# Kernel tuning notes

Hardware: AMD Instinct MI355X
Metric: run time of the kernel (lower is better)

The kernel has to match this reference:

```python
import jax, jax.numpy as jnp
import numpy as np

TOP_K = 2


def setup_inputs() -> dict:
    key = jax.random.key(0)
    k_x, k_g, k_w1, k_w2, k_w3 = jax.random.split(key, 5)
    B, S, D, H, E = 2, 512, 1024, 512, 8
    x = jax.random.normal(k_x, (B, S, D), dtype=jnp.float32)
    gate_w = jax.random.normal(k_g, (D, E), dtype=jnp.float32) * (D ** -0.5)
    w1 = jax.random.normal(k_w1, (E, D, H), dtype=jnp.float32) * 0.02  # gate proj
    w2 = jax.random.normal(k_w2, (E, H, D), dtype=jnp.float32) * 0.02  # down proj
    w3 = jax.random.normal(k_w3, (E, D, H), dtype=jnp.float32) * 0.02  # up proj
    return {"x": x, "gate_w": gate_w, "w1": w1, "w2": w2, "w3": w3}


def reference(x, gate_w, w1, w2, w3):
    # Token-choice top-k MoE with grouped SwiGLU experts, no shared expert.
    # Equivalent to torchtune MoE: gather routed tokens, scale by top-k router
    # score, run per-expert FFN, scatter-add back. Since each expert's FFN has
    # no bias (FFN(0) == 0), the dispatch/grouped-GEMM/combine is expressed
    # densely as sum_e FFN_e(scale[:, e] * x), which is mathematically identical.
    B, S, D = x.shape
    E = gate_w.shape[1]
    xf = x.reshape(B * S, D)                      # [T, D]
    T = B * S

    logits = xf @ gate_w                          # [T, E]
    scores = jax.nn.softmax(logits, axis=-1)
    top_scores, top_idx = jax.lax.top_k(scores, TOP_K)  # [T, k]

    # scale[t, e] = router score if expert e selected for token t, else 0
    scale = jnp.zeros((T, E), dtype=x.dtype).at[
        jnp.arange(T)[:, None], top_idx
    ].set(top_scores)

    xs = scale.T[:, :, None] * xf[None, :, :]     # [E, T, D] scaled routed input
    h = jax.nn.silu(jnp.einsum('etd,edh->eth', xs, w1)) \
        * jnp.einsum('etd,edh->eth', xs, w3)      # [E, T, H]
    y = jnp.einsum('eth,ehd->etd', h, w2)         # [E, T, D]
    out = y.sum(axis=0)                           # combine (scatter-add equiv)
    return out.reshape(B, S, D)
```

## Files before the change

### kernel.cpp

```cpp
#include <hip/hip_runtime.h>
#include <hip/hip_bf16.h>
#include <cstddef>

#define T_TOK 1024
#define D_DIM 1024
#define H_DIM 512
#define E_EXP 8
#define P_CAP 2560
#define MAX_MT 72
#define LDA 72

typedef __attribute__((ext_vector_type(4))) float    float4_t;
typedef __attribute__((ext_vector_type(8))) short    short8_t;
typedef __attribute__((ext_vector_type(4))) unsigned uint4_t;

__device__ __forceinline__ short f2bf(float f) {
  union { float f; unsigned u; } v; v.f = f;
  unsigned u = v.u;
  u += 0x7FFFu + ((u >> 16) & 1u);
  return (short)(u >> 16);
}

__device__ __forceinline__ unsigned pkbf(float a, float b) {
  union { __hip_bfloat162 h; unsigned u; } v;
  v.h = __float22bfloat162_rn(make_float2(a, b));
  return v.u;
}

__global__ __launch_bounds__(256) void prep_kernel(
    const float* __restrict__ w1, const float* __restrict__ w3,
    const float* __restrict__ w2, const float* __restrict__ x,
    const float* __restrict__ gw, short* __restrict__ w13t,
    short* __restrict__ w2t, int* __restrict__ idx2,
    float* __restrict__ scale2, float* __restrict__ out) {
  __shared__ float tile[64][69];
  const int z = blockIdx.z;
  const int tid = threadIdx.x;

  if (z < 24) {
    const float* src; short* dst; int N, ldd, row_off;
    if (z < 16) {
      if (blockIdx.y >= 8) return;
      int which = z >> 3, e = z & 7;
      src = (which ? w3 : w1) + (size_t)e * D_DIM * H_DIM;
      dst = w13t + (size_t)e * D_DIM * (2 * H_DIM);
      N = H_DIM; ldd = D_DIM; row_off = which ? H_DIM : 0;
    } else {
      if (blockIdx.x >= 8) return;
      int e = z - 16;
      src = w2 + (size_t)e * H_DIM * D_DIM;
      dst = w2t + (size_t)e * D_DIM * H_DIM;
      N = D_DIM; ldd = H_DIM; row_off = 0;
    }
    const int k0 = blockIdx.x * 64, n0 = blockIdx.y * 64;
    const int kr = tid >> 4, nc = (tid & 15) * 4;
    #pragma unroll
    for (int p = 0; p < 4; ++p) {
      int k = p * 16 + kr;
      float4_t v = *(const float4_t*)(src + (size_t)(k0 + k) * N + n0 + nc);
      tile[k][nc]     = v[0];
      tile[k][nc + 1] = v[1];
      tile[k][nc + 2] = v[2];
      tile[k][nc + 3] = v[3];
    }
    __syncthreads();
    const int r8 = tid >> 3, c8 = tid & 7;
    #pragma unroll
    for (int p = 0; p < 2; ++p) {
      int row = p * 32 + r8;
      uint4_t u;
      #pragma unroll
      for (int jj = 0; jj < 4; ++jj)
        u[jj] = pkbf(tile[c8 * 8 + 2 * jj][row], tile[c8 * 8 + 2 * jj + 1][row]);
      *(uint4_t*)(dst + (size_t)(row_off + n0 + row) * ldd + k0 + c8 * 8) = u;
    }
    return;
  }

  if (z == 25) {
    float4_t z4 = {0.f, 0.f, 0.f, 0.f};
    float4_t* o = (float4_t*)(out + ((size_t)(blockIdx.y * 16 + blockIdx.x)) * 4096);
    #pragma unroll
    for (int i = 0; i < 4; ++i) o[i * 256 + tid] = z4;
    return;
  }

  const int wid  = tid >> 6;
  const int lane = tid & 63;
  const int t = (blockIdx.y * 16 + blockIdx.x) * 4 + wid;
  const float* xr = x + (size_t)t * D_DIM;
  float acc[E_EXP];
  #pragma unroll
  for (int e = 0; e < E_EXP; ++e) acc[e] = 0.f;
  for (int d = lane; d < D_DIM; d += 64) {
    float xv = xr[d];
    float4_t g0 = *(const float4_t*)(gw + d * E_EXP);
    float4_t g1 = *(const float4_t*)(gw + d * E_EXP + 4);
    acc[0] += xv * g0[0]; acc[1] += xv * g0[1];
    acc[2] += xv * g0[2]; acc[3] += xv * g0[3];
    acc[4] += xv * g1[0]; acc[5] += xv * g1[1];
    acc[6] += xv * g1[2]; acc[7] += xv * g1[3];
  }
  #pragma unroll
  for (int off = 32; off >= 1; off >>= 1) {
    #pragma unroll
    for (int e = 0; e < E_EXP; ++e) acc[e] += __shfl_down(acc[e], off, 64);
  }
  if (lane == 0) {
    float m = acc[0];
    #pragma unroll
    for (int e = 1; e < E_EXP; ++e) m = fmaxf(m, acc[e]);
    float p[E_EXP]; float s = 0.f;
    #pragma unroll
    for (int e = 0; e < E_EXP; ++e) { p[e] = __expf(acc[e] - m); s += p[e]; }
    float inv = 1.f / s;
    #pragma unroll
    for (int e = 0; e < E_EXP; ++e) p[e] *= inv;
    int i1 = 0;
    #pragma unroll
    for (int e = 1; e < E_EXP; ++e) if (p[e] > p[i1]) i1 = e;
    int i2 = (i1 == 0) ? 1 : 0;
    #pragma unroll
    for (int e = 0; e < E_EXP; ++e) {
      if (e == i1 || e == i2) continue;
      if (p[e] > p[i2]) i2 = e;
    }
    idx2[2 * t]     = i1;  scale2[2 * t]     = p[i1];
    idx2[2 * t + 1] = i2;  scale2[2 * t + 1] = p[i2];
  }
}

__global__ __launch_bounds__(256) void scan_kernel(
    const int* __restrict__ idx2, const float* __restrict__ scale2,
    int* __restrict__ pair_tok, float* __restrict__ pair_scale,
    int* __restrict__ meta) {
  __shared__ int cnt[E_EXP], base[E_EXP], cur[E_EXP];
  const int tid = threadIdx.x;
  if (tid < E_EXP) { cnt[tid] = 0; cur[tid] = 0; }
  for (int p = tid; p < P_CAP; p += 256) { pair_tok[p] = -1; pair_scale[p] = 0.f; }
  __syncthreads();
  for (int t = tid; t < T_TOK; t += 256) {
    atomicAdd(&cnt[idx2[2 * t]], 1);
    atomicAdd(&cnt[idx2[2 * t + 1]], 1);
  }
  __syncthreads();
  if (tid == 0) {
    int b = 0, g = 0;
    for (int e = 0; e < E_EXP; ++e) {
      base[e] = b;
      int al = (cnt[e] + 31) & ~31;
      for (int j = 0; j < al; j += 32) { meta[1 + g] = e; meta[81 + g] = b + j; ++g; }
      b += al;
    }
    meta[0] = g;
  }
  __syncthreads();
  for (int t = tid; t < T_TOK; t += 256) {
    #pragma unroll
    for (int s = 0; s < 2; ++s) {
      int e = idx2[2 * t + s];
      int p = base[e] + atomicAdd(&cur[e], 1);
      pair_tok[p] = t;
      pair_scale[p] = scale2[2 * t + s];
    }
  }
}

__global__ __launch_bounds__(256, 6) void gemm1_kernel(
    const float* __restrict__ x, const short* __restrict__ w13t,
    const int* __restrict__ pair_tok, const float* __restrict__ pair_scale,
    const int* __restrict__ meta, short* __restrict__ h) {
  __shared__ short As[32 * LDA];
  __shared__ short B1s[32 * LDA];
  __shared__ short B3s[32 * LDA];
  const int mt = blockIdx.y;
  if (mt >= meta[0]) return;
  const int e    = meta[1 + mt];
  const int row0 = meta[81 + mt];
  const int n0   = blockIdx.x * 32;
  const int tid = threadIdx.x, lane = tid & 63, wid = tid >> 6;
  const int wr = wid >> 1, wc = wid & 1;
  const int q = lane >> 4, ln = lane & 15;
  const short* bsrc = w13t + (size_t)e * D_DIM * (2 * H_DIM);

  const int ar = tid >> 3, ak = (tid & 7) * 8;
  const int   tokr = pair_tok[row0 + ar];
  const float sc   = pair_scale[row0 + ar];
  const float* xrow = x + (size_t)(tokr < 0 ? 0 : tokr) * D_DIM + ak;
  const int br = tid >> 3, bu = (tid & 7) * 8;
  const short* b1p = bsrc + (size_t)(n0 + br) * D_DIM + bu;
  const short* b3p = bsrc + (size_t)(H_DIM + n0 + br) * D_DIM + bu;

  float4_t acc1 = {0.f, 0.f, 0.f, 0.f}, acc3 = {0.f, 0.f, 0.f, 0.f};

  for (int k0 = 0; k0 < D_DIM; k0 += 64) {
    float4_t v0 = *(const float4_t*)(xrow + k0);
    float4_t v1 = *(const float4_t*)(xrow + k0 + 4);
    uint4_t vb1 = *(const uint4_t*)(b1p + k0);
    uint4_t vb3 = *(const uint4_t*)(b3p + k0);
    uint4_t u0 = {pkbf(v0[0] * sc, v0[1] * sc), pkbf(v0[2] * sc, v0[3] * sc),
                  pkbf(v1[0] * sc, v1[1] * sc), pkbf(v1[2] * sc, v1[3] * sc)};
    *(uint4_t*)&As[ar * LDA + ak]  = u0;
    *(uint4_t*)&B1s[br * LDA + bu] = vb1;
    *(uint4_t*)&B3s[br * LDA + bu] = vb3;
    __syncthreads();

    short8_t af[2], b1f[2], b3f[2];
    #pragma unroll
    for (int kk = 0; kk < 2; ++kk) {
      af[kk]  = *(const short8_t*)&As[(wr * 16 + ln) * LDA + kk * 32 + q * 8];
      b1f[kk] = *(const short8_t*)&B1s[(wc * 16 + ln) * LDA + kk * 32 + q * 8];
      b3f[kk] = *(const short8_t*)&B3s[(wc * 16 + ln) * LDA + kk * 32 + q * 8];
    }
    #pragma unroll
    for (int kk = 0; kk < 2; ++kk) {
      acc1 = __builtin_amdgcn_mfma_f32_16x16x32_bf16(af[kk], b1f[kk], acc1, 0, 0, 0);
      acc3 = __builtin_amdgcn_mfma_f32_16x16x32_bf16(af[kk], b3f[kk], acc3, 0, 0, 0);
    }
    __syncthreads();
  }

  {
    int r_base = row0 + wr * 16 + q * 4;
    int col = n0 + wc * 16 + ln;
    #pragma unroll
    for (int rr = 0; rr < 4; ++rr) {
      float c1 = acc1[rr];
      float c3 = acc3[rr];
      float sig = 1.f / (1.f + __expf(-c1));
      h[(size_t)(r_base + rr) * H_DIM + col] = f2bf(c1 * sig * c3);
    }
  }
}

__global__ __launch_bounds__(256, 6) void gemm2_kernel(
    const short* __restrict__ h, const short* __restrict__ w2t,
    const int* __restrict__ pair_tok, const int* __restrict__ meta,
    float* __restrict__ out) {
  __shared__ short As[32 * LDA];
  __shared__ short Bs[64 * LDA];
  const int mt = blockIdx.y;
  if (mt >= meta[0]) return;
  const int e    = meta[1 + mt];
  const int row0 = meta[81 + mt];
  const int n0   = blockIdx.x * 64;
  const int tid = threadIdx.x, lane = tid & 63, wid = tid >> 6;
  const int wr = wid >> 1, wc = wid & 1;
  const int q = lane >> 4, ln = lane & 15;
  const short* bsrc = w2t + (size_t)e * D_DIM * H_DIM;

  const int ar = tid >> 3, ak = (tid & 7) * 8;
  const short* arow = h + (size_t)(row0 + ar) * H_DIM + ak;
  const int br = tid >> 2, bk = (tid & 3) * 16;
  const short* brow = bsrc + (size_t)(n0 + br) * H_DIM + bk;

  float4_t acc[2];
  acc[0] = acc[1] = (float4_t){0.f, 0.f, 0.f, 0.f};

  for (int k0 = 0; k0 < H_DIM; k0 += 64) {
    uint4_t va  = *(const uint4_t*)(arow + k0);
    uint4_t vb0 = *(const uint4_t*)(brow + k0);
    uint4_t vb1 = *(const uint4_t*)(brow + k0 + 8);
    *(uint4_t*)&As[ar * LDA + ak]     = va;
    *(uint4_t*)&Bs[br * LDA + bk]     = vb0;
    *(uint4_t*)&Bs[br * LDA + bk + 8] = vb1;
    __syncthreads();

    short8_t af[2], bf[2][2];
    #pragma unroll
    for (int kk = 0; kk < 2; ++kk) {
      af[kk] = *(const short8_t*)&As[(wr * 16 + ln) * LDA + kk * 32 + q * 8];
      #pragma unroll
      for (int j = 0; j < 2; ++j)
        bf[j][kk] = *(const short8_t*)&Bs[(wc * 32 + j * 16 + ln) * LDA + kk * 32 + q * 8];
    }
    #pragma unroll
    for (int j = 0; j < 2; ++j)
      #pragma unroll
      for (int kk = 0; kk < 2; ++kk)
        acc[j] = __builtin_amdgcn_mfma_f32_16x16x32_bf16(af[kk], bf[j][kk], acc[j], 0, 0, 0);
    __syncthreads();
  }

  {
    int r_base = row0 + wr * 16 + q * 4;
    #pragma unroll
    for (int rr = 0; rr < 4; ++rr) {
      int tok = pair_tok[r_base + rr];
      if (tok < 0) continue;
      float* orow = out + (size_t)tok * D_DIM;
      #pragma unroll
      for (int j = 0; j < 2; ++j) {
        int col = n0 + wc * 32 + j * 16 + ln;
        atomicAdd(orow + col, acc[j][rr]);
      }
    }
  }
}

extern "C" void kernel_launch(void* const* d_in, const int* in_sizes, int n_in,
                              void* d_out, int out_size, void* d_ws, size_t ws_size,
                              hipStream_t stream) {
  const float* x  = (const float*)d_in[0];
  const float* gw = (const float*)d_in[1];
  const float* w1 = (const float*)d_in[2];
  const float* w2 = (const float*)d_in[3];
  const float* w3 = (const float*)d_in[4];
  float* out = (float*)d_out;

  char* ws = (char*)d_ws;
  int*   idx2    = (int*)  (ws);
  float* scale2  = (float*)(ws + 8192);
  int*   ptok    = (int*)  (ws + 16384);
  float* pscale  = (float*)(ws + 32768);
  int*   meta    = (int*)  (ws + 49152);
  short* h       = (short*)(ws + (1u << 20));
  short* w13t    = (short*)(ws + (4u << 20));
  short* w2t     = (short*)(ws + (21u << 20));

  prep_kernel<<<dim3(16, 16, 26), dim3(256), 0, stream>>>(
      w1, w3, w2, x, gw, w13t, w2t, idx2, scale2, out);
  scan_kernel<<<dim3(1), dim3(256), 0, stream>>>(idx2, scale2, ptok, pscale, meta);
  gemm1_kernel<<<dim3(H_DIM / 32, MAX_MT), dim3(256), 0, stream>>>(
      x, w13t, ptok, pscale, meta, h);
  gemm2_kernel<<<dim3(D_DIM / 64, MAX_MT), dim3(256), 0, stream>>>(
      h, w2t, ptok, meta, out);
}
```

Baseline: 146.9 us.

## Drop LDS staging in expert GEMMs and load MFMA fragments directly from global

```diff
diff --git a/kernel.cpp b/kernel.cpp
--- a/kernel.cpp
+++ b/kernel.cpp
@@ -8,7 +8,6 @@
 #define E_EXP 8
 #define P_CAP 2560
 #define MAX_MT 72
-#define LDA 72
 
 typedef __attribute__((ext_vector_type(4))) float    float4_t;
 typedef __attribute__((ext_vector_type(8))) short    short8_t;
@@ -166,13 +165,10 @@
   }
 }
 
-__global__ __launch_bounds__(256, 6) void gemm1_kernel(
+__global__ __launch_bounds__(256, 4) void gemm1_kernel(
     const float* __restrict__ x, const short* __restrict__ w13t,
     const int* __restrict__ pair_tok, const float* __restrict__ pair_scale,
     const int* __restrict__ meta, short* __restrict__ h) {
-  __shared__ short As[32 * LDA];
-  __shared__ short B1s[32 * LDA];
-  __shared__ short B3s[32 * LDA];
   const int mt = blockIdx.y;
   if (mt >= meta[0]) return;
   const int e    = meta[1 + mt];
@@ -181,120 +177,77 @@
   const int tid = threadIdx.x, lane = tid & 63, wid = tid >> 6;
   const int wr = wid >> 1, wc = wid & 1;
   const int q = lane >> 4, ln = lane & 15;
+
+  const int   mrow = row0 + wr * 16 + ln;
+  const int   tokr = pair_tok[mrow];
+  const float sc   = pair_scale[mrow];
+  const float* ap  = x + (size_t)(tokr < 0 ? 0 : tokr) * D_DIM + q * 8;
+
+  const int ncol = n0 + wc * 16 + ln;
   const short* bsrc = w13t + (size_t)e * D_DIM * (2 * H_DIM);
-
-  const int ar = tid >> 3, ak = (tid & 7) * 8;
-  const int   tokr = pair_tok[row0 + ar];
-  const float sc   = pair_scale[row0 + ar];
-  const float* xrow = x + (size_t)(tokr < 0 ? 0 : tokr) * D_DIM + ak;
-  const int br = tid >> 3, bu = (tid & 7) * 8;
-  const short* b1p = bsrc + (size_t)(n0 + br) * D_DIM + bu;
-  const short* b3p = bsrc + (size_t)(H_DIM + n0 + br) * D_DIM + bu;
+  const short* b1p = bsrc + (size_t)ncol * D_DIM + q * 8;
+  const short* b3p = bsrc + (size_t)(H_DIM + ncol) * D_DIM + q * 8;
 
   float4_t acc1 = {0.f, 0.f, 0.f, 0.f}, acc3 = {0.f, 0.f, 0.f, 0.f};
 
-  for (int k0 = 0; k0 < D_DIM; k0 += 64) {
-    float4_t v0 = *(const float4_t*)(xrow + k0);
-    float4_t v1 = *(const float4_t*)(xrow + k0 + 4);
-    uint4_t vb1 = *(const uint4_t*)(b1p + k0);
-    uint4_t vb3 = *(const uint4_t*)(b3p + k0);
-    uint4_t u0 = {pkbf(v0[0] * sc, v0[1] * sc), pkbf(v0[2] * sc, v0[3] * sc),
+  #pragma unroll 4
+  for (int k0 = 0; k0 < D_DIM; k0 += 32) {
+    float4_t v0 = *(const float4_t*)(ap + k0);
+    float4_t v1 = *(const float4_t*)(ap + k0 + 4);
+    short8_t b1 = *(const short8_t*)(b1p + k0);
+    short8_t b3 = *(const short8_t*)(b3p + k0);
+    uint4_t ua = {pkbf(v0[0] * sc, v0[1] * sc), pkbf(v0[2] * sc, v0[3] * sc),
                   pkbf(v1[0] * sc, v1[1] * sc), pkbf(v1[2] * sc, v1[3] * sc)};
-    *(uint4_t*)&As[ar * LDA + ak]  = u0;
-    *(uint4_t*)&B1s[br * LDA + bu] = vb1;
-    *(uint4_t*)&B3s[br * LDA + bu] = vb3;
-    __syncthreads();
-
-    short8_t af[2], b1f[2], b3f[2];
-    #pragma unroll
-    for (int kk = 0; kk < 2; ++kk) {
-      af[kk]  = *(const short8_t*)&As[(wr * 16 + ln) * LDA + kk * 32 + q * 8];
-      b1f[kk] = *(const short8_t*)&B1s[(wc * 16 + ln) * LDA + kk * 32 + q * 8];
-      b3f[kk] = *(const short8_t*)&B3s[(wc * 16 + ln) * LDA + kk * 32 + q * 8];
-    }
-    #pragma unroll
-    for (int kk = 0; kk < 2; ++kk) {
-      acc1 = __builtin_amdgcn_mfma_f32_16x16x32_bf16(af[kk], b1f[kk], acc1, 0, 0, 0);
-      acc3 = __builtin_amdgcn_mfma_f32_16x16x32_bf16(af[kk], b3f[kk], acc3, 0, 0, 0);
-    }
-    __syncthreads();
-  }
-
-  {
-    int r_base = row0 + wr * 16 + q * 4;
-    int col = n0 + wc * 16 + ln;
-    #pragma unroll
-    for (int rr = 0; rr < 4; ++rr) {
-      float c1 = acc1[rr];
-      float c3 = acc3[rr];
-      float sig = 1.f / (1.f + __expf(-c1));
-      h[(size_t)(r_base + rr) * H_DIM + col] = f2bf(c1 * sig * c3);
-    }
-  }
-}
-
-__global__ __launch_bounds__(256, 6) void gemm2_kernel(
+    short8_t af = *(short8_t*)&ua;
+    acc1 = __builtin_amdgcn_mfma_f32_16x16x32_bf16(af, b1, acc1, 0, 0, 0);
+    acc3 = __builtin_amdgcn_mfma_f32_16x16x32_bf16(af, b3, acc3, 0, 0, 0);
+  }
+
+  const int r_base = row0 + wr * 16 + q * 4;
+  const int col = n0 + wc * 16 + ln;
+  #pragma unroll
+  for (int rr = 0; rr < 4; ++rr) {
+    float c1 = acc1[rr];
+    float c3 = acc3[rr];
+    float sig = 1.f / (1.f + __expf(-c1));
+    h[(size_t)(r_base + rr) * H_DIM + col] = f2bf(c1 * sig * c3);
+  }
+}
+
+__global__ __launch_bounds__(256, 8) void gemm2_kernel(
     const short* __restrict__ h, const short* __restrict__ w2t,
     const int* __restrict__ pair_tok, const int* __restrict__ meta,
     float* __restrict__ out) {
-  __shared__ short As[32 * LDA];
-  __shared__ short Bs[64 * LDA];
   const int mt = blockIdx.y;
   if (mt >= meta[0]) return;
   const int e    = meta[1 + mt];
   const int row0 = meta[81 + mt];
-  const int n0   = blockIdx.x * 64;
+  const int n0   = blockIdx.x * 32;
   const int tid = threadIdx.x, lane = tid & 63, wid = tid >> 6;
   const int wr = wid >> 1, wc = wid & 1;
   const int q = lane >> 4, ln = lane & 15;
-  const short* bsrc = w2t + (size_t)e * D_DIM * H_DIM;
-
-  const int ar = tid >> 3, ak = (tid & 7) * 8;
-  const short* arow = h + (size_t)(row0 + ar) * H_DIM + ak;
-  const int br = tid >> 2, bk = (tid & 3) * 16;
-  const short* brow = bsrc + (size_t)(n0 + br) * H_DIM + bk;
-
-  float4_t acc[2];
-  acc[0] = acc[1] = (float4_t){0.f, 0.f, 0.f, 0.f};
-
-  for (int k0 = 0; k0 < H_DIM; k0 += 64) {
-    uint4_t va  = *(const uint4_t*)(arow + k0);
-    uint4_t vb0 = *(const uint4_t*)(brow + k0);
-    uint4_t vb1 = *(const uint4_t*)(brow + k0 + 8);
-    *(uint4_t*)&As[ar * LDA + ak]     = va;
-    *(uint4_t*)&Bs[br * LDA + bk]     = vb0;
-    *(uint4_t*)&Bs[br * LDA + bk + 8] = vb1;
-    __syncthreads();
-
-    short8_t af[2], bf[2][2];
-    #pragma unroll
-    for (int kk = 0; kk < 2; ++kk) {
-      af[kk] = *(const short8_t*)&As[(wr * 16 + ln) * LDA + kk * 32 + q * 8];
-      #pragma unroll
-      for (int j = 0; j < 2; ++j)
-        bf[j][kk] = *(const short8_t*)&Bs[(wc * 32 + j * 16 + ln) * LDA + kk * 32 + q * 8];
-    }
-    #pragma unroll
-    for (int j = 0; j < 2; ++j)
-      #pragma unroll
-      for (int kk = 0; kk < 2; ++kk)
-        acc[j] = __builtin_amdgcn_mfma_f32_16x16x32_bf16(af[kk], bf[j][kk], acc[j], 0, 0, 0);
-    __syncthreads();
-  }
-
-  {
-    int r_base = row0 + wr * 16 + q * 4;
-    #pragma unroll
-    for (int rr = 0; rr < 4; ++rr) {
-      int tok = pair_tok[r_base + rr];
-      if (tok < 0) continue;
-      float* orow = out + (size_t)tok * D_DIM;
-      #pragma unroll
-      for (int j = 0; j < 2; ++j) {
-        int col = n0 + wc * 32 + j * 16 + ln;
-        atomicAdd(orow + col, acc[j][rr]);
-      }
-    }
+
+  const int mrow = row0 + wr * 16 + ln;
+  const short* arow = h + (size_t)mrow * H_DIM + q * 8;
+  const int ncol = n0 + wc * 16 + ln;
+  const short* bp = w2t + (size_t)e * D_DIM * H_DIM + (size_t)ncol * H_DIM + q * 8;
+
+  float4_t acc = {0.f, 0.f, 0.f, 0.f};
+
+  #pragma unroll 4
+  for (int k0 = 0; k0 < H_DIM; k0 += 32) {
+    short8_t af = *(const short8_t*)(arow + k0);
+    short8_t bf = *(const short8_t*)(bp + k0);
+    acc = __builtin_amdgcn_mfma_f32_16x16x32_bf16(af, bf, acc, 0, 0, 0);
+  }
+
+  const int r_base = row0 + wr * 16 + q * 4;
+  const int col = n0 + wc * 16 + ln;
+  #pragma unroll
+  for (int rr = 0; rr < 4; ++rr) {
+    int tok = pair_tok[r_base + rr];
+    if (tok < 0) continue;
+    atomicAdd(out + (size_t)tok * D_DIM + col, acc[rr]);
   }
 }
 
@@ -323,6 +276,6 @@
   scan_kernel<<<dim3(1), dim3(256), 0, stream>>>(idx2, scale2, ptok, pscale, meta);
   gemm1_kernel<<<dim3(H_DIM / 32, MAX_MT), dim3(256), 0, stream>>>(
       x, w13t, ptok, pscale, meta, h);
-  gemm2_kernel<<<dim3(D_DIM / 64, MAX_MT), dim3(256), 0, stream>>>(
+  gemm2_kernel<<<dim3(D_DIM / 32, MAX_MT), dim3(256), 0, stream>>>(
       h, w2t, ptok, meta, out);
 }
```

After: 223.7 us. 52.2% more time.

## Drop weight pre-transpose pass; convert and transpose fp32 weights inside GEMM tile loads

Applied to the files above, without the earlier changes.

```diff
diff --git a/kernel.cpp b/kernel.cpp
--- a/kernel.cpp
+++ b/kernel.cpp
@@ -9,10 +9,12 @@
 #define P_CAP 2560
 #define MAX_MT 72
 #define LDA 72
+#define LDAW 36
 
 typedef __attribute__((ext_vector_type(4))) float    float4_t;
 typedef __attribute__((ext_vector_type(8))) short    short8_t;
 typedef __attribute__((ext_vector_type(4))) unsigned uint4_t;
+typedef __attribute__((ext_vector_type(2))) unsigned uint2_t;
 
 __device__ __forceinline__ short f2bf(float f) {
   union { float f; unsigned u; } v; v.f = f;
@@ -28,58 +30,15 @@
 }
 
 __global__ __launch_bounds__(256) void prep_kernel(
-    const float* __restrict__ w1, const float* __restrict__ w3,
-    const float* __restrict__ w2, const float* __restrict__ x,
-    const float* __restrict__ gw, short* __restrict__ w13t,
-    short* __restrict__ w2t, int* __restrict__ idx2,
-    float* __restrict__ scale2, float* __restrict__ out) {
-  __shared__ float tile[64][69];
-  const int z = blockIdx.z;
+    const float* __restrict__ x, const float* __restrict__ gw,
+    int* __restrict__ idx2, float* __restrict__ scale2,
+    float* __restrict__ out) {
+  const int bid = blockIdx.x;
   const int tid = threadIdx.x;
 
-  if (z < 24) {
-    const float* src; short* dst; int N, ldd, row_off;
-    if (z < 16) {
-      if (blockIdx.y >= 8) return;
-      int which = z >> 3, e = z & 7;
-      src = (which ? w3 : w1) + (size_t)e * D_DIM * H_DIM;
-      dst = w13t + (size_t)e * D_DIM * (2 * H_DIM);
-      N = H_DIM; ldd = D_DIM; row_off = which ? H_DIM : 0;
-    } else {
-      if (blockIdx.x >= 8) return;
-      int e = z - 16;
-      src = w2 + (size_t)e * H_DIM * D_DIM;
-      dst = w2t + (size_t)e * D_DIM * H_DIM;
-      N = D_DIM; ldd = H_DIM; row_off = 0;
-    }
-    const int k0 = blockIdx.x * 64, n0 = blockIdx.y * 64;
-    const int kr = tid >> 4, nc = (tid & 15) * 4;
-    #pragma unroll
-    for (int p = 0; p < 4; ++p) {
-      int k = p * 16 + kr;
-      float4_t v = *(const float4_t*)(src + (size_t)(k0 + k) * N + n0 + nc);
-      tile[k][nc]     = v[0];
-      tile[k][nc + 1] = v[1];
-      tile[k][nc + 2] = v[2];
-      tile[k][nc + 3] = v[3];
-    }
-    __syncthreads();
-    const int r8 = tid >> 3, c8 = tid & 7;
-    #pragma unroll
-    for (int p = 0; p < 2; ++p) {
-      int row = p * 32 + r8;
-      uint4_t u;
-      #pragma unroll
-      for (int jj = 0; jj < 4; ++jj)
-        u[jj] = pkbf(tile[c8 * 8 + 2 * jj][row], tile[c8 * 8 + 2 * jj + 1][row]);
-      *(uint4_t*)(dst + (size_t)(row_off + n0 + row) * ldd + k0 + c8 * 8) = u;
-    }
-    return;
-  }
-
-  if (z == 25) {
+  if (bid < 256) {
     float4_t z4 = {0.f, 0.f, 0.f, 0.f};
-    float4_t* o = (float4_t*)(out + ((size_t)(blockIdx.y * 16 + blockIdx.x)) * 4096);
+    float4_t* o = (float4_t*)(out + (size_t)bid * 4096);
     #pragma unroll
     for (int i = 0; i < 4; ++i) o[i * 256 + tid] = z4;
     return;
@@ -87,7 +46,7 @@
 
   const int wid  = tid >> 6;
   const int lane = tid & 63;
-  const int t = (blockIdx.y * 16 + blockIdx.x) * 4 + wid;
+  const int t = (bid - 256) * 4 + wid;
   const float* xr = x + (size_t)t * D_DIM;
   float acc[E_EXP];
   #pragma unroll
@@ -167,7 +126,8 @@
 }
 
 __global__ __launch_bounds__(256, 6) void gemm1_kernel(
-    const float* __restrict__ x, const short* __restrict__ w13t,
+    const float* __restrict__ x, const float* __restrict__ w1,
+    const float* __restrict__ w3,
     const int* __restrict__ pair_tok, const float* __restrict__ pair_scale,
     const int* __restrict__ meta, short* __restrict__ h) {
   __shared__ short As[32 * LDA];
@@ -181,28 +141,39 @@
   const int tid = threadIdx.x, lane = tid & 63, wid = tid >> 6;
   const int wr = wid >> 1, wc = wid & 1;
   const int q = lane >> 4, ln = lane & 15;
-  const short* bsrc = w13t + (size_t)e * D_DIM * (2 * H_DIM);
+  const float* w1e = w1 + (size_t)e * D_DIM * H_DIM;
+  const float* w3e = w3 + (size_t)e * D_DIM * H_DIM;
 
   const int ar = tid >> 3, ak = (tid & 7) * 8;
   const int   tokr = pair_tok[row0 + ar];
   const float sc   = pair_scale[row0 + ar];
   const float* xrow = x + (size_t)(tokr < 0 ? 0 : tokr) * D_DIM + ak;
-  const int br = tid >> 3, bu = (tid & 7) * 8;
-  const short* b1p = bsrc + (size_t)(n0 + br) * D_DIM + bu;
-  const short* b3p = bsrc + (size_t)(H_DIM + n0 + br) * D_DIM + bu;
+  const int kd = tid >> 3;
+  const int n4 = (tid & 7) * 4;
+  const float* b1p = w1e + (size_t)(2 * kd) * H_DIM + n0 + n4;
+  const float* b3p = w3e + (size_t)(2 * kd) * H_DIM + n0 + n4;
+  unsigned* B1w = (unsigned*)B1s;
+  unsigned* B3w = (unsigned*)B3s;
 
   float4_t acc1 = {0.f, 0.f, 0.f, 0.f}, acc3 = {0.f, 0.f, 0.f, 0.f};
 
   for (int k0 = 0; k0 < D_DIM; k0 += 64) {
     float4_t v0 = *(const float4_t*)(xrow + k0);
     float4_t v1 = *(const float4_t*)(xrow + k0 + 4);
-    uint4_t vb1 = *(const uint4_t*)(b1p + k0);
-    uint4_t vb3 = *(const uint4_t*)(b3p + k0);
+    const float* bk1 = b1p + (size_t)k0 * H_DIM;
+    const float* bk3 = b3p + (size_t)k0 * H_DIM;
+    float4_t a0 = *(const float4_t*)(bk1);
+    float4_t a1 = *(const float4_t*)(bk1 + H_DIM);
+    float4_t c0 = *(const float4_t*)(bk3);
+    float4_t c1 = *(const float4_t*)(bk3 + H_DIM);
     uint4_t u0 = {pkbf(v0[0] * sc, v0[1] * sc), pkbf(v0[2] * sc, v0[3] * sc),
                   pkbf(v1[0] * sc, v1[1] * sc), pkbf(v1[2] * sc, v1[3] * sc)};
-    *(uint4_t*)&As[ar * LDA + ak]  = u0;
-    *(uint4_t*)&B1s[br * LDA + bu] = vb1;
-    *(uint4_t*)&B3s[br * LDA + bu] = vb3;
+    *(uint4_t*)&As[ar * LDA + ak] = u0;
+    #pragma unroll
+    for (int i = 0; i < 4; ++i) {
+      B1w[(n4 + i) * LDAW + kd] = pkbf(a0[i], a1[i]);
+      B3w[(n4 + i) * LDAW + kd] = pkbf(c0[i], c1[i]);
+    }
     __syncthreads();
 
     short8_t af[2], b1f[2], b3f[2];
@@ -234,7 +205,7 @@
 }
 
 __global__ __launch_bounds__(256, 6) void gemm2_kernel(
-    const short* __restrict__ h, const short* __restrict__ w2t,
+    const short* __restrict__ h, const float* __restrict__ w2,
     const int* __restrict__ pair_tok, const int* __restrict__ meta,
     float* __restrict__ out) {
   __shared__ short As[32 * LDA];
@@ -247,23 +218,31 @@
   const int tid = threadIdx.x, lane = tid & 63, wid = tid >> 6;
   const int wr = wid >> 1, wc = wid & 1;
   const int q = lane >> 4, ln = lane & 15;
-  const short* bsrc = w2t + (size_t)e * D_DIM * H_DIM;
+  const float* w2e = w2 + (size_t)e * H_DIM * D_DIM;
 
   const int ar = tid >> 3, ak = (tid & 7) * 8;
   const short* arow = h + (size_t)(row0 + ar) * H_DIM + ak;
-  const int br = tid >> 2, bk = (tid & 3) * 16;
-  const short* brow = bsrc + (size_t)(n0 + br) * H_DIM + bk;
+  const int kq = tid >> 4;
+  const int n4 = (tid & 15) * 4;
+  const float* bp = w2e + (size_t)(4 * kq) * D_DIM + n0 + n4;
+  unsigned* Bw = (unsigned*)Bs;
 
   float4_t acc[2];
   acc[0] = acc[1] = (float4_t){0.f, 0.f, 0.f, 0.f};
 
   for (int k0 = 0; k0 < H_DIM; k0 += 64) {
-    uint4_t va  = *(const uint4_t*)(arow + k0);
-    uint4_t vb0 = *(const uint4_t*)(brow + k0);
-    uint4_t vb1 = *(const uint4_t*)(brow + k0 + 8);
-    *(uint4_t*)&As[ar * LDA + ak]     = va;
-    *(uint4_t*)&Bs[br * LDA + bk]     = vb0;
-    *(uint4_t*)&Bs[br * LDA + bk + 8] = vb1;
+    uint4_t va = *(const uint4_t*)(arow + k0);
+    const float* bk = bp + (size_t)k0 * D_DIM;
+    float4_t r0 = *(const float4_t*)(bk);
+    float4_t r1 = *(const float4_t*)(bk + D_DIM);
+    float4_t r2 = *(const float4_t*)(bk + 2 * D_DIM);
+    float4_t r3 = *(const float4_t*)(bk + 3 * D_DIM);
+    *(uint4_t*)&As[ar * LDA + ak] = va;
+    #pragma unroll
+    for (int i = 0; i < 4; ++i) {
+      uint2_t u = {pkbf(r0[i], r1[i]), pkbf(r2[i], r3[i])};
+      *(uint2_t*)&Bw[(n4 + i) * LDAW + kq * 2] = u;
+    }
     __syncthreads();
 
     short8_t af[2], bf[2][2];
@@ -315,14 +294,11 @@
   float* pscale  = (float*)(ws + 32768);
   int*   meta    = (int*)  (ws + 49152);
   short* h       = (short*)(ws + (1u << 20));
-  short* w13t    = (short*)(ws + (4u << 20));
-  short* w2t     = (short*)(ws + (21u << 20));
-
-  prep_kernel<<<dim3(16, 16, 26), dim3(256), 0, stream>>>(
-      w1, w3, w2, x, gw, w13t, w2t, idx2, scale2, out);
+
+  prep_kernel<<<dim3(512), dim3(256), 0, stream>>>(x, gw, idx2, scale2, out);
   scan_kernel<<<dim3(1), dim3(256), 0, stream>>>(idx2, scale2, ptok, pscale, meta);
   gemm1_kernel<<<dim3(H_DIM / 32, MAX_MT), dim3(256), 0, stream>>>(
-      x, w13t, ptok, pscale, meta, h);
+      x, w1, w3, ptok, pscale, meta, h);
   gemm2_kernel<<<dim3(D_DIM / 64, MAX_MT), dim3(256), 0, stream>>>(
-      h, w2t, ptok, meta, out);
-}
+      h, w2, ptok, meta, out);
+}
```

Result: slower. 153.1 us (+4.2%).
